# Optimization experiments

Hardware: AMD Instinct MI355X
Metric: run time of the kernel (lower is better)

Reference implementation:

```python
import jax, jax.numpy as jnp
import numpy as np

N_NODES = 50000
N_EDGES = 100000
N_RELS = 64
D_IN = 64
D_OUT = 64


def setup_inputs() -> dict:
    key = jax.random.key(0)
    k1, k2, k3, k4, k5, k6 = jax.random.split(key, 6)
    h = jax.random.normal(k1, (N_NODES, D_IN), dtype=jnp.float32)
    src = jax.random.randint(k2, (N_EDGES,), 0, N_NODES)
    rel = jax.random.randint(k3, (N_EDGES,), 0, N_RELS)
    dst = jax.random.randint(k4, (N_EDGES,), 0, N_NODES)
    edges = jnp.stack([src, rel, dst], axis=1)
    # xavier_uniform with gain for relu: bound = gain * sqrt(6 / (fan_in + fan_out))
    gain = float(np.sqrt(2.0))
    bound = gain * float(np.sqrt(6.0 / (D_IN + D_OUT)))
    weight = jax.random.uniform(k5, (N_RELS, D_IN, D_OUT), dtype=jnp.float32,
                                minval=-bound, maxval=bound)
    self_loop_weight = jax.random.uniform(k6, (D_IN, D_OUT), dtype=jnp.float32,
                                          minval=-bound, maxval=bound)
    return {"h": h, "edges": edges, "weight": weight,
            "self_loop_weight": self_loop_weight}


def reference(h, edges, weight, self_loop_weight):
    # h: (N, D_IN); edges: (E, 3) int columns (src, rel, dst)
    src, rel, dst = edges[:, 0], edges[:, 1], edges[:, 2]
    n_nodes = h.shape[0]
    n_edges = src.shape[0]

    # per-edge relation-specific transform: (E,1,in) bmm (E,in,out) -> (E,out)
    src_h = h[src]                                    # (E, D_IN)
    msg = jnp.einsum('ei,eio->eo', src_h, weight[rel])  # (E, D_OUT)

    # -> last edge index per destination node
    last_edge = jax.ops.segment_max(jnp.arange(n_edges, dtype=jnp.int32), dst,
                                    num_segments=n_nodes)  # (N,)
    # msg = msg[index_matrix[dst]]: every edge to node d takes the msg of the
    # last edge pointing to d
    msg = msg[last_edge[dst]]                          # (E, D_OUT)

    # scatter-mean aggregate over dst (only nodes with incoming edges updated)
    sums = jax.ops.segment_sum(msg, dst, num_segments=n_nodes)          # (N, D_OUT)
    counts = jax.ops.segment_sum(jnp.ones((n_edges,), h.dtype), dst,
                                 num_segments=n_nodes)                   # (N,)
    has_in = counts > 0
    agg = jnp.where(has_in[:, None],
                    sums / jnp.maximum(counts, 1.0)[:, None], 0.0)

    out = h @ self_loop_weight                         # (N, D_OUT)
    return out + agg
```

## Files before the change

### kernel.cpp

```cpp
#include <hip/hip_runtime.h>

#define NN 50000
#define NE 100000
#define NREL 64
#define D 64
#define RCAP 1280
#define SCAP 8192
#define CSTR 16
#define BR   8
#define SBLK 64
#define FILL_BLOCKS 128
#define FILL_ITERS  2

typedef unsigned long long u64;
using f16x8 = __attribute__((ext_vector_type(8))) _Float16;
using f32x4 = __attribute__((ext_vector_type(4))) float;

#define WS_CURSOR  (512 * 1024)
#define WS_RBUCKET (520 * 1024)
#define WS_SBUCKET (896 * 1024)
#define WS_H2      (1024 * 1024)

struct H4 { _Float16 v[4]; };

__global__ __launch_bounds__(256) void k_pre(
    const float* __restrict__ h, u64* __restrict__ packed,
    int* __restrict__ cursor, _Float16* __restrict__ h2)
{
    const int t = blockIdx.x * 256 + threadIdx.x;
    const int nthr = gridDim.x * 256;
    for (int i = t; i < NN; i += nthr) packed[i] = 0ull;
    if (t < 65) cursor[t * CSTR] = 0;

    const float4* __restrict__ hf4 = reinterpret_cast<const float4*>(h);
    H4* __restrict__ o4 = reinterpret_cast<H4*>(h2);
    for (int m = t; m < NN * (D / 4); m += nthr) {
        const float4 p = hf4[m];
        H4 o;
        o.v[0] = (_Float16)p.x; o.v[1] = (_Float16)p.y;
        o.v[2] = (_Float16)p.z; o.v[3] = (_Float16)p.w;
        o4[m] = o;
    }
}

__global__ void k_scatter(const int* __restrict__ edges, u64* __restrict__ packed) {
    int e = blockIdx.x * blockDim.x + threadIdx.x;
    if (e < NE) {
        int s = edges[e * 3 + 0];
        int r = edges[e * 3 + 1];
        int d = edges[e * 3 + 2];
        u64 key = ((u64)(e + 1) << 22) | ((u64)r << 16) | (u64)s;
        atomicMax(&packed[d], key);
    }
}

__global__ __launch_bounds__(256) void k_fill(
    const u64* __restrict__ packed, int* __restrict__ cursor,
    unsigned* __restrict__ rbucket, unsigned* __restrict__ sbucket)
{
    __shared__ int hcnt[65];
    __shared__ int hbase[65];
    const int t = threadIdx.x;
    if (t < 65) hcnt[t] = 0;
    __syncthreads();

    int      myr[FILL_ITERS];
    int      myslot[FILL_ITERS];
    unsigned myent[FILL_ITERS];

    #pragma unroll
    for (int it = 0; it < FILL_ITERS; ++it) {
        const int v = (blockIdx.x * FILL_ITERS + it) * 256 + t;
        myr[it] = -1;
        if (v < NN) {
            u64 key = packed[v];
            if (key) {
                myr[it]   = (int)((key >> 16) & 63);
                myent[it] = ((unsigned)v << 16) | (unsigned)(key & 0xFFFF);
            } else {
                myr[it]   = 64;
                myent[it] = (unsigned)v;
            }
            myslot[it] = atomicAdd(&hcnt[myr[it]], 1);
        }
    }
    __syncthreads();
    if (t < 65 && hcnt[t] > 0)
        hbase[t] = atomicAdd(&cursor[t * CSTR], hcnt[t]);
    __syncthreads();

    #pragma unroll
    for (int it = 0; it < FILL_ITERS; ++it) {
        const int r = myr[it];
        if (r >= 0) {
            const int p = hbase[r] + myslot[it];
            if (r < 64) { if (p < RCAP) rbucket[r * RCAP + p] = myent[it]; }
            else        { if (p < SCAP) sbucket[p] = myent[it]; }
        }
    }
}

__global__ __launch_bounds__(256) void k_compute(
    const _Float16* __restrict__ h2, const float* __restrict__ weight,
    const float* __restrict__ wself, const unsigned* __restrict__ rbucket,
    const unsigned* __restrict__ sbucket, const int* __restrict__ cursor,
    float* __restrict__ out)
{
    __shared__ _Float16 lds_w[D * D];
    __shared__ _Float16 lds_ws[D * D];

    const int lane = threadIdx.x & 63;
    const int wv   = threadIdx.x >> 6;
    const bool isRel = blockIdx.x < NREL * BR;

    int r = 64, wslot, wstride, cnt;
    const unsigned* __restrict__ seg;
    if (isRel) {
        r = blockIdx.x / BR;
        wslot = (blockIdx.x % BR) * 4 + wv;
        wstride = BR * 4;
        seg = rbucket + r * RCAP;
        cnt = min(cursor[r * CSTR], RCAP);
    } else {
        wslot = (blockIdx.x - NREL * BR) * 4 + wv;
        wstride = SBLK * 4;
        seg = sbucket;
        cnt = min(cursor[64 * CSTR], SCAP);
    }
    if (cnt == 0) return;

    if (isRel) {
        const float4* __restrict__ W4 = reinterpret_cast<const float4*>(weight + (size_t)r * D * D);
        for (int i = threadIdx.x; i < D * D / 4; i += 256) {
            const float4 w = W4[i];
            H4 o; o.v[0]=(_Float16)w.x; o.v[1]=(_Float16)w.y; o.v[2]=(_Float16)w.z; o.v[3]=(_Float16)w.w;
            *reinterpret_cast<H4*>(&lds_w[i * 4]) = o;
        }
    }
    {
        const float4* __restrict__ WS4 = reinterpret_cast<const float4*>(wself);
        for (int i = threadIdx.x; i < D * D / 4; i += 256) {
            const float4 w = WS4[i];
            H4 o; o.v[0]=(_Float16)w.x; o.v[1]=(_Float16)w.y; o.v[2]=(_Float16)w.z; o.v[3]=(_Float16)w.w;
            *reinterpret_cast<H4*>(&lds_ws[i * 4]) = o;
        }
    }
    __syncthreads();

    const int kbase = (lane >> 4) * 8;
    const int ncol  = lane & 15;

    f16x8 bws[4][2];
    #pragma unroll
    for (int nt = 0; nt < 4; ++nt)
        #pragma unroll
        for (int ks = 0; ks < 2; ++ks) {
            f16x8 f;
            #pragma unroll
            for (int j = 0; j < 8; ++j)
                f[j] = lds_ws[(ks * 32 + kbase + j) * D + nt * 16 + ncol];
            bws[nt][ks] = f;
        }

    f16x8 bw[4][2];
    if (isRel) {
        #pragma unroll
        for (int nt = 0; nt < 4; ++nt)
            #pragma unroll
            for (int ks = 0; ks < 2; ++ks) {
                f16x8 f;
                #pragma unroll
                for (int j = 0; j < 8; ++j)
                    f[j] = lds_w[(ks * 32 + kbase + j) * D + nt * 16 + ncol];
                bw[nt][ks] = f;
            }
    }

    for (int t = wslot; t * 16 < cnt; t += wstride) {
        const int myidx = min(t * 16 + ncol, cnt - 1);
        const unsigned ent = seg[myidx];
        const int v = isRel ? (int)(ent >> 16) : (int)ent;
        const int s = (int)(ent & 0xFFFF);

        f32x4 c[4];
        #pragma unroll
        for (int nt = 0; nt < 4; ++nt) c[nt] = (f32x4){0.f, 0.f, 0.f, 0.f};

        {
            const f16x8 a0 = *reinterpret_cast<const f16x8*>(h2 + (size_t)v * D + kbase);
            const f16x8 a1 = *reinterpret_cast<const f16x8*>(h2 + (size_t)v * D + 32 + kbase);
            #pragma unroll
            for (int nt = 0; nt < 4; ++nt) {
                c[nt] = __builtin_amdgcn_mfma_f32_16x16x32_f16(a0, bws[nt][0], c[nt], 0, 0, 0);
                c[nt] = __builtin_amdgcn_mfma_f32_16x16x32_f16(a1, bws[nt][1], c[nt], 0, 0, 0);
            }
        }
        if (isRel) {
            const f16x8 a0 = *reinterpret_cast<const f16x8*>(h2 + (size_t)s * D + kbase);
            const f16x8 a1 = *reinterpret_cast<const f16x8*>(h2 + (size_t)s * D + 32 + kbase);
            #pragma unroll
            for (int nt = 0; nt < 4; ++nt) {
                c[nt] = __builtin_amdgcn_mfma_f32_16x16x32_f16(a0, bw[nt][0], c[nt], 0, 0, 0);
                c[nt] = __builtin_amdgcn_mfma_f32_16x16x32_f16(a1, bw[nt][1], c[nt], 0, 0, 0);
            }
        }

        int vrow[4];
        #pragma unroll
        for (int q = 0; q < 4; ++q)
            vrow[q] = __shfl(v, (lane >> 4) * 4 + q, 64);

        #pragma unroll
        for (int nt = 0; nt < 4; ++nt)
            #pragma unroll
            for (int q = 0; q < 4; ++q)
                out[(size_t)vrow[q] * D + nt * 16 + ncol] = c[nt][q];
    }
}

extern "C" void kernel_launch(void* const* d_in, const int* in_sizes, int n_in,
                              void* d_out, int out_size, void* d_ws, size_t ws_size,
                              hipStream_t stream) {
    const float* h      = (const float*)d_in[0];
    const int*   edges  = (const int*)d_in[1];
    const float* weight = (const float*)d_in[2];
    const float* wself  = (const float*)d_in[3];
    float* out = (float*)d_out;

    char* ws = (char*)d_ws;
    u64*      packed  = (u64*)ws;
    int*      cursor  = (int*)(ws + WS_CURSOR);
    unsigned* rbucket = (unsigned*)(ws + WS_RBUCKET);
    unsigned* sbucket = (unsigned*)(ws + WS_SBUCKET);
    _Float16* h2      = (_Float16*)(ws + WS_H2);

    k_pre<<<512, 256, 0, stream>>>(h, packed, cursor, h2);
    k_scatter<<<(NE + 255) / 256, 256, 0, stream>>>(edges, packed);
    k_fill<<<FILL_BLOCKS, 256, 0, stream>>>(packed, cursor, rbucket, sbucket);
    k_compute<<<NREL * BR + SBLK, 256, 0, stream>>>(h2, weight, wself, rbucket, sbucket, cursor, out);
}
```

Baseline: 33.17 us.

## Fuse dense self-loop GEMM with edge scatter and drop fp16 h staging

Drops the separate fp16 conversion pass over h. Activations are now converted to fp16 in registers as they are loaded. The self-loop GEMM runs for every node inside the same launch as the atomic edge scatter. Bucket filling now iterates over edges, keeping only each destination's winning edge, and no longer scans all nodes. The relation kernel recomputes the self-loop term and overwrites those rows. This saves one full read/write of h and the no-incoming bucket, at the cost of redundant self-loop work for nodes with incoming edges and fp32 gathers of h.

```diff
diff --git a/kernel.cpp b/kernel.cpp
--- a/kernel.cpp
+++ b/kernel.cpp
@@ -5,138 +5,55 @@
 #define NREL 64
 #define D 64
 #define RCAP 1280
-#define SCAP 8192
 #define CSTR 16
 #define BR   8
-#define SBLK 64
-#define FILL_BLOCKS 128
-#define FILL_ITERS  2
+#define SC_BLK ((NE + 255) / 256)
+#define DN_BLK 782
 
 typedef unsigned long long u64;
 using f16x8 = __attribute__((ext_vector_type(8))) _Float16;
 using f32x4 = __attribute__((ext_vector_type(4))) float;
 
-#define WS_CURSOR  (512 * 1024)
-#define WS_RBUCKET (520 * 1024)
-#define WS_SBUCKET (896 * 1024)
-#define WS_H2      (1024 * 1024)
+#define WS_CURSOR  (400 * 1024)
+#define WS_RBUCKET (408 * 1024)
 
 struct H4 { _Float16 v[4]; };
 
-__global__ __launch_bounds__(256) void k_pre(
-    const float* __restrict__ h, u64* __restrict__ packed,
-    int* __restrict__ cursor, _Float16* __restrict__ h2)
-{
+__global__ __launch_bounds__(256) void k_zero(u64* __restrict__ packed, int* __restrict__ cursor) {
     const int t = blockIdx.x * 256 + threadIdx.x;
     const int nthr = gridDim.x * 256;
     for (int i = t; i < NN; i += nthr) packed[i] = 0ull;
-    if (t < 65) cursor[t * CSTR] = 0;
-
-    const float4* __restrict__ hf4 = reinterpret_cast<const float4*>(h);
-    H4* __restrict__ o4 = reinterpret_cast<H4*>(h2);
-    for (int m = t; m < NN * (D / 4); m += nthr) {
-        const float4 p = hf4[m];
-        H4 o;
-        o.v[0] = (_Float16)p.x; o.v[1] = (_Float16)p.y;
-        o.v[2] = (_Float16)p.z; o.v[3] = (_Float16)p.w;
-        o4[m] = o;
-    }
-}
-
-__global__ void k_scatter(const int* __restrict__ edges, u64* __restrict__ packed) {
-    int e = blockIdx.x * blockDim.x + threadIdx.x;
-    if (e < NE) {
-        int s = edges[e * 3 + 0];
-        int r = edges[e * 3 + 1];
-        int d = edges[e * 3 + 2];
-        u64 key = ((u64)(e + 1) << 22) | ((u64)r << 16) | (u64)s;
-        atomicMax(&packed[d], key);
-    }
-}
-
-__global__ __launch_bounds__(256) void k_fill(
-    const u64* __restrict__ packed, int* __restrict__ cursor,
-    unsigned* __restrict__ rbucket, unsigned* __restrict__ sbucket)
-{
-    __shared__ int hcnt[65];
-    __shared__ int hbase[65];
-    const int t = threadIdx.x;
-    if (t < 65) hcnt[t] = 0;
-    __syncthreads();
-
-    int      myr[FILL_ITERS];
-    int      myslot[FILL_ITERS];
-    unsigned myent[FILL_ITERS];
-
-    #pragma unroll
-    for (int it = 0; it < FILL_ITERS; ++it) {
-        const int v = (blockIdx.x * FILL_ITERS + it) * 256 + t;
-        myr[it] = -1;
-        if (v < NN) {
-            u64 key = packed[v];
-            if (key) {
-                myr[it]   = (int)((key >> 16) & 63);
-                myent[it] = ((unsigned)v << 16) | (unsigned)(key & 0xFFFF);
-            } else {
-                myr[it]   = 64;
-                myent[it] = (unsigned)v;
-            }
-            myslot[it] = atomicAdd(&hcnt[myr[it]], 1);
-        }
-    }
-    __syncthreads();
-    if (t < 65 && hcnt[t] > 0)
-        hbase[t] = atomicAdd(&cursor[t * CSTR], hcnt[t]);
-    __syncthreads();
-
-    #pragma unroll
-    for (int it = 0; it < FILL_ITERS; ++it) {
-        const int r = myr[it];
-        if (r >= 0) {
-            const int p = hbase[r] + myslot[it];
-            if (r < 64) { if (p < RCAP) rbucket[r * RCAP + p] = myent[it]; }
-            else        { if (p < SCAP) sbucket[p] = myent[it]; }
-        }
-    }
-}
-
-__global__ __launch_bounds__(256) void k_compute(
-    const _Float16* __restrict__ h2, const float* __restrict__ weight,
-    const float* __restrict__ wself, const unsigned* __restrict__ rbucket,
-    const unsigned* __restrict__ sbucket, const int* __restrict__ cursor,
+    if (t < 64) cursor[t * CSTR] = 0;
+}
+
+__device__ __forceinline__ f16x8 cvt_frag(const float* __restrict__ p) {
+    const float4 p0 = *reinterpret_cast<const float4*>(p);
+    const float4 p1 = *reinterpret_cast<const float4*>(p + 4);
+    f16x8 a;
+    a[0] = (_Float16)p0.x; a[1] = (_Float16)p0.y; a[2] = (_Float16)p0.z; a[3] = (_Float16)p0.w;
+    a[4] = (_Float16)p1.x; a[5] = (_Float16)p1.y; a[6] = (_Float16)p1.z; a[7] = (_Float16)p1.w;
+    return a;
+}
+
+__global__ __launch_bounds__(256) void k_scatdense(
+    const int* __restrict__ edges, const float* __restrict__ h,
+    const float* __restrict__ wself, u64* __restrict__ packed,
     float* __restrict__ out)
 {
-    __shared__ _Float16 lds_w[D * D];
     __shared__ _Float16 lds_ws[D * D];
 
-    const int lane = threadIdx.x & 63;
-    const int wv   = threadIdx.x >> 6;
-    const bool isRel = blockIdx.x < NREL * BR;
-
-    int r = 64, wslot, wstride, cnt;
-    const unsigned* __restrict__ seg;
-    if (isRel) {
-        r = blockIdx.x / BR;
-        wslot = (blockIdx.x % BR) * 4 + wv;
-        wstride = BR * 4;
-        seg = rbucket + r * RCAP;
-        cnt = min(cursor[r * CSTR], RCAP);
-    } else {
-        wslot = (blockIdx.x - NREL * BR) * 4 + wv;
-        wstride = SBLK * 4;
-        seg = sbucket;
-        cnt = min(cursor[64 * CSTR], SCAP);
-    }
-    if (cnt == 0) return;
-
-    if (isRel) {
-        const float4* __restrict__ W4 = reinterpret_cast<const float4*>(weight + (size_t)r * D * D);
-        for (int i = threadIdx.x; i < D * D / 4; i += 256) {
-            const float4 w = W4[i];
-            H4 o; o.v[0]=(_Float16)w.x; o.v[1]=(_Float16)w.y; o.v[2]=(_Float16)w.z; o.v[3]=(_Float16)w.w;
-            *reinterpret_cast<H4*>(&lds_w[i * 4]) = o;
-        }
-    }
+    if (blockIdx.x < SC_BLK) {
+        const int e = blockIdx.x * 256 + threadIdx.x;
+        if (e < NE) {
+            const int s = edges[e * 3 + 0];
+            const int r = edges[e * 3 + 1];
+            const int d = edges[e * 3 + 2];
+            const u64 key = ((u64)(e + 1) << 22) | ((u64)r << 16) | (u64)s;
+            atomicMax(&packed[d], key);
+        }
+        return;
+    }
+
     {
         const float4* __restrict__ WS4 = reinterpret_cast<const float4*>(wself);
         for (int i = threadIdx.x; i < D * D / 4; i += 256) {
@@ -147,6 +64,8 @@
     }
     __syncthreads();
 
+    const int lane = threadIdx.x & 63;
+    const int wv   = threadIdx.x >> 6;
     const int kbase = (lane >> 4) * 8;
     const int ncol  = lane & 15;
 
@@ -162,54 +81,128 @@
             bws[nt][ks] = f;
         }
 
-    f16x8 bw[4][2];
-    if (isRel) {
-        #pragma unroll
-        for (int nt = 0; nt < 4; ++nt)
+    const int tt = (blockIdx.x - SC_BLK) * 4 + wv;
+    if (tt * 16 >= NN) return;
+    const int v = min(tt * 16 + ncol, NN - 1);
+
+    const float* __restrict__ hv = h + (size_t)v * D;
+    const f16x8 a0 = cvt_frag(hv + kbase);
+    const f16x8 a1 = cvt_frag(hv + 32 + kbase);
+
+    f32x4 c[4];
+    #pragma unroll
+    for (int nt = 0; nt < 4; ++nt) c[nt] = (f32x4){0.f, 0.f, 0.f, 0.f};
+    #pragma unroll
+    for (int nt = 0; nt < 4; ++nt) {
+        c[nt] = __builtin_amdgcn_mfma_f32_16x16x32_f16(a0, bws[nt][0], c[nt], 0, 0, 0);
+        c[nt] = __builtin_amdgcn_mfma_f32_16x16x32_f16(a1, bws[nt][1], c[nt], 0, 0, 0);
+    }
+
+    int vrow[4];
+    #pragma unroll
+    for (int q = 0; q < 4; ++q)
+        vrow[q] = __shfl(v, (lane >> 4) * 4 + q, 64);
+    #pragma unroll
+    for (int nt = 0; nt < 4; ++nt)
+        #pragma unroll
+        for (int q = 0; q < 4; ++q)
+            out[(size_t)vrow[q] * D + nt * 16 + ncol] = c[nt][q];
+}
+
+__global__ __launch_bounds__(256) void k_fille(
+    const int* __restrict__ edges, const u64* __restrict__ packed,
+    int* __restrict__ cursor, unsigned* __restrict__ rbucket)
+{
+    const int e = blockIdx.x * 256 + threadIdx.x;
+    if (e < NE) {
+        const int d = edges[e * 3 + 2];
+        const u64 key = packed[d];
+        if ((int)(key >> 22) == e + 1) {
+            const int r = (int)((key >> 16) & 63);
+            const int p = atomicAdd(&cursor[r * CSTR], 1);
+            if (p < RCAP)
+                rbucket[r * RCAP + p] = ((unsigned)d << 16) | (unsigned)(key & 0xFFFF);
+        }
+    }
+}
+
+__global__ __launch_bounds__(256) void k_rel(
+    const float* __restrict__ h, const float* __restrict__ weight,
+    const float* __restrict__ wself, const unsigned* __restrict__ rbucket,
+    const int* __restrict__ cursor, float* __restrict__ out)
+{
+    __shared__ _Float16 lds_w[D * D];
+    __shared__ _Float16 lds_ws[D * D];
+
+    const int lane = threadIdx.x & 63;
+    const int wv   = threadIdx.x >> 6;
+    const int r     = blockIdx.x / BR;
+    const int wslot = (blockIdx.x % BR) * 4 + wv;
+    const int cnt   = min(cursor[r * CSTR], RCAP);
+    if (cnt == 0) return;
+
+    {
+        const float4* __restrict__ W4 = reinterpret_cast<const float4*>(weight + (size_t)r * D * D);
+        const float4* __restrict__ WS4 = reinterpret_cast<const float4*>(wself);
+        for (int i = threadIdx.x; i < D * D / 4; i += 256) {
+            const float4 w = W4[i];
+            H4 o; o.v[0]=(_Float16)w.x; o.v[1]=(_Float16)w.y; o.v[2]=(_Float16)w.z; o.v[3]=(_Float16)w.w;
+            *reinterpret_cast<H4*>(&lds_w[i * 4]) = o;
+            const float4 u = WS4[i];
+            H4 p; p.v[0]=(_Float16)u.x; p.v[1]=(_Float16)u.y; p.v[2]=(_Float16)u.z; p.v[3]=(_Float16)u.w;
+            *reinterpret_cast<H4*>(&lds_ws[i * 4]) = p;
+        }
+    }
+    __syncthreads();
+
+    const int kbase = (lane >> 4) * 8;
+    const int ncol  = lane & 15;
+
+    f16x8 bw[4][2], bws[4][2];
+    #pragma unroll
+    for (int nt = 0; nt < 4; ++nt)
+        #pragma unroll
+        for (int ks = 0; ks < 2; ++ks) {
+            f16x8 f, g;
             #pragma unroll
-            for (int ks = 0; ks < 2; ++ks) {
-                f16x8 f;
-                #pragma unroll
-                for (int j = 0; j < 8; ++j)
-                    f[j] = lds_w[(ks * 32 + kbase + j) * D + nt * 16 + ncol];
-                bw[nt][ks] = f;
+            for (int j = 0; j < 8; ++j) {
+                f[j] = lds_w [(ks * 32 + kbase + j) * D + nt * 16 + ncol];
+                g[j] = lds_ws[(ks * 32 + kbase + j) * D + nt * 16 + ncol];
             }
-    }
-
-    for (int t = wslot; t * 16 < cnt; t += wstride) {
-        const int myidx = min(t * 16 + ncol, cnt - 1);
-        const unsigned ent = seg[myidx];
-        const int v = isRel ? (int)(ent >> 16) : (int)ent;
+            bw[nt][ks] = f;
+            bws[nt][ks] = g;
+        }
+
+    const unsigned* __restrict__ seg = rbucket + r * RCAP;
+
+    for (int t = wslot; t * 16 < cnt; t += BR * 4) {
+        const unsigned ent = seg[min(t * 16 + ncol, cnt - 1)];
+        const int v = (int)(ent >> 16);
         const int s = (int)(ent & 0xFFFF);
 
+        const float* __restrict__ hv = h + (size_t)v * D;
+        const float* __restrict__ hs = h + (size_t)s * D;
+        const f16x8 a0 = cvt_frag(hv + kbase);
+        const f16x8 a1 = cvt_frag(hv + 32 + kbase);
+        const f16x8 s0 = cvt_frag(hs + kbase);
+        const f16x8 s1 = cvt_frag(hs + 32 + kbase);
+
         f32x4 c[4];
         #pragma unroll
         for (int nt = 0; nt < 4; ++nt) c[nt] = (f32x4){0.f, 0.f, 0.f, 0.f};
 
-        {
-            const f16x8 a0 = *reinterpret_cast<const f16x8*>(h2 + (size_t)v * D + kbase);
-            const f16x8 a1 = *reinterpret_cast<const f16x8*>(h2 + (size_t)v * D + 32 + kbase);
-            #pragma unroll
-            for (int nt = 0; nt < 4; ++nt) {
-                c[nt] = __builtin_amdgcn_mfma_f32_16x16x32_f16(a0, bws[nt][0], c[nt], 0, 0, 0);
-                c[nt] = __builtin_amdgcn_mfma_f32_16x16x32_f16(a1, bws[nt][1], c[nt], 0, 0, 0);
-            }
-        }
-        if (isRel) {
-            const f16x8 a0 = *reinterpret_cast<const f16x8*>(h2 + (size_t)s * D + kbase);
-            const f16x8 a1 = *reinterpret_cast<const f16x8*>(h2 + (size_t)s * D + 32 + kbase);
-            #pragma unroll
-            for (int nt = 0; nt < 4; ++nt) {
-                c[nt] = __builtin_amdgcn_mfma_f32_16x16x32_f16(a0, bw[nt][0], c[nt], 0, 0, 0);
-                c[nt] = __builtin_amdgcn_mfma_f32_16x16x32_f16(a1, bw[nt][1], c[nt], 0, 0, 0);
-            }
+        #pragma unroll
+        for (int nt = 0; nt < 4; ++nt) {
+            c[nt] = __builtin_amdgcn_mfma_f32_16x16x32_f16(a0, bws[nt][0], c[nt], 0, 0, 0);
+            c[nt] = __builtin_amdgcn_mfma_f32_16x16x32_f16(a1, bws[nt][1], c[nt], 0, 0, 0);
+            c[nt] = __builtin_amdgcn_mfma_f32_16x16x32_f16(s0, bw[nt][0],  c[nt], 0, 0, 0);
+            c[nt] = __builtin_amdgcn_mfma_f32_16x16x32_f16(s1, bw[nt][1],  c[nt], 0, 0, 0);
         }
 
         int vrow[4];
         #pragma unroll
         for (int q = 0; q < 4; ++q)
             vrow[q] = __shfl(v, (lane >> 4) * 4 + q, 64);
-
         #pragma unroll
         for (int nt = 0; nt < 4; ++nt)
             #pragma unroll
@@ -231,11 +224,9 @@
     u64*      packed  = (u64*)ws;
     int*      cursor  = (int*)(ws + WS_CURSOR);
     unsigned* rbucket = (unsigned*)(ws + WS_RBUCKET);
-    unsigned* sbucket = (unsigned*)(ws + WS_SBUCKET);
-    _Float16* h2      = (_Float16*)(ws + WS_H2);
-
-    k_pre<<<512, 256, 0, stream>>>(h, packed, cursor, h2);
-    k_scatter<<<(NE + 255) / 256, 256, 0, stream>>>(edges, packed);
-    k_fill<<<FILL_BLOCKS, 256, 0, stream>>>(packed, cursor, rbucket, sbucket);
-    k_compute<<<NREL * BR + SBLK, 256, 0, stream>>>(h2, weight, wself, rbucket, sbucket, cursor, out);
-}
+
+    k_zero<<<98, 256, 0, stream>>>(packed, cursor);
+    k_scatdense<<<SC_BLK + DN_BLK, 256, 0, stream>>>(edges, h, wself, packed, out);
+    k_fille<<<SC_BLK, 256, 0, stream>>>(edges, packed, cursor, rbucket);
+    k_rel<<<NREL * BR, 256, 0, stream>>>(h, weight, wself, rbucket, cursor, out);
+}
```

New measurement: 47.03 us. 41.8% more time.
